# Kernel tuning notes

Hardware: AMD Instinct MI355X
Metric: run time of the kernel (lower is better)

## Reference

```python
import jax, jax.numpy as jnp
import numpy as np

N, E = 50000, 800000
IN_DIM = OUT_DIM = 256
T, R, H = 4, 8, 8
DK = OUT_DIM // H


def typed_linear(x, node_type, W, b):
    # per-node-type linear: small fixed loop over T types, select via mask
    out = jnp.zeros((x.shape[0], W.shape[2]), dtype=x.dtype)
    for t in range(W.shape[0]):
        y = x @ W[t] + b[t]
        out = jnp.where((node_type == t)[:, None], y, out)
    return out


def setup_inputs() -> dict:
    key = jax.random.key(0)
    ks = jax.random.split(key, 16)
    x = jax.random.normal(ks[0], (N, IN_DIM), dtype=jnp.float32)
    node_type = jax.random.randint(ks[1], (N,), 0, T, dtype=jnp.int32)
    src = jax.random.randint(ks[2], (E,), 0, N, dtype=jnp.int32)
    # every node receives E//N incoming edges (original skips message-less nodes)
    dst = (jnp.arange(E, dtype=jnp.int32) % N)
    etype = jax.random.randint(ks[3], (E,), 0, R, dtype=jnp.int32)
    w_scale = np.sqrt(2.0 / (IN_DIM + OUT_DIM)).astype(np.float32)
    r_scale = np.sqrt(2.0 / (DK + DK)).astype(np.float32)
    def lin(k):
        return jax.random.normal(k, (T, IN_DIM, OUT_DIM), dtype=jnp.float32) * w_scale
    return {
        "x": x, "node_type": node_type, "src": src, "dst": dst, "etype": etype,
        "Wk": lin(ks[4]), "bk": jnp.zeros((T, OUT_DIM), jnp.float32),
        "Wq": lin(ks[5]), "bq": jnp.zeros((T, OUT_DIM), jnp.float32),
        "Wv": lin(ks[6]), "bv": jnp.zeros((T, OUT_DIM), jnp.float32),
        "Wa": lin(ks[7]), "ba": jnp.zeros((T, OUT_DIM), jnp.float32),
        "rel_att": jax.random.normal(ks[8], (R, H, DK, DK), jnp.float32) * r_scale,
        "rel_msg": jax.random.normal(ks[9], (R, H, DK, DK), jnp.float32) * r_scale,
        "rel_pri": jnp.ones((R, H), jnp.float32),
        "skip": jnp.ones((T,), jnp.float32),
    }


def reference(x, node_type, src, dst, etype, Wk, bk, Wq, bq, Wv, bv, Wa, ba,
              rel_att, rel_msg, rel_pri, skip):
    n = x.shape[0]
    r = rel_att.shape[0]
    h, dk = rel_att.shape[1], rel_att.shape[2]
    sqrt_dk = jnp.asarray(np.sqrt(dk), x.dtype)

    # per-node-type K/Q/V projections -> [N, H, DK]
    k = typed_linear(x, node_type, Wk, bk).reshape(n, h, dk)
    q = typed_linear(x, node_type, Wq, bq).reshape(n, h, dk)
    v = typed_linear(x, node_type, Wv, bv).reshape(n, h, dk)

    # relation-specific transforms at node granularity: [R, N, H, DK]
    k_r = jnp.einsum('nhd,rhde->rnhe', k, rel_att)
    v_r = jnp.einsum('nhd,rhde->rnhe', v, rel_msg)

    # per-edge attention logits and messages (gather, no dense adjacency)
    key_e = k_r[etype, src]                  # [E, H, DK]
    val_e = v_r[etype, src]                  # [E, H, DK]
    att = (q[dst] * key_e).sum(-1) * rel_pri[etype] / sqrt_dk   # [E, H]

    # ragged softmax per (dst node, etype) segment, like DGL mailbox per etype
    seg = dst * r + etype
    s = n * r
    m = jax.ops.segment_max(att, seg, num_segments=s)           # [S, H]
    ex = jnp.exp(att - m[seg])
    den = jax.ops.segment_sum(ex, seg, num_segments=s)
    alpha = ex / den[seg]                                       # [E, H]
    hmsg = jax.ops.segment_sum(alpha[..., None] * val_e, seg, num_segments=s)
    hmsg = hmsg.reshape(n, r, h * dk)                           # [N, R, OUT]

    # cross_reducer='mean' over relation types that actually delivered messages
    cnt = jax.ops.segment_sum(jnp.ones((att.shape[0],), x.dtype), seg, num_segments=s)
    present = (cnt.reshape(n, r) > 0).astype(x.dtype)           # [N, R]
    t = hmsg.sum(1) / jnp.maximum(present.sum(1, keepdims=True), 1.0)

    # per-type output projection + sigmoid skip gate (dropout=identity in eval)
    trans = typed_linear(t, node_type, Wa, ba)
    a = jax.nn.sigmoid(skip)[node_type][:, None]
    return trans * a + x * (1.0 - a)
```

## Files before the change

kernel.cpp:

```cpp
#include <hip/hip_runtime.h>

#define TT 4
#define RR 8
#define NH 8
#define DKK 32

typedef float floatx4 __attribute__((ext_vector_type(4)));
typedef __bf16 bf16x8 __attribute__((ext_vector_type(8)));

__device__ __forceinline__ float us2f(unsigned short s){
    union{unsigned int u; float f;} x; x.u = ((unsigned int)s) << 16; return x.f;
}
__device__ __forceinline__ float lo2f(unsigned int u){
    union{unsigned int x; float f;} a; a.x = u << 16; return a.f;
}
__device__ __forceinline__ float hi2f(unsigned int u){
    union{unsigned int x; float f;} a; a.x = u & 0xffff0000u; return a.f;
}
__device__ __forceinline__ unsigned short f2us(float f){
    union{float f; unsigned int u;} x; x.f = f;
    unsigned int u = x.u;
    unsigned int r = (u + 0x7fffu + ((u >> 16) & 1u)) >> 16;
    return (unsigned short)r;
}
__device__ __forceinline__ float ldf(const void* p, int i, int isf32){
    return isf32 ? ((const float*)p)[i] : us2f(((const unsigned short*)p)[i]);
}
__device__ __forceinline__ float4 ldf4(const void* p, int i, int isf32){
    if (isf32) return *reinterpret_cast<const float4*>((const float*)p + i);
    uint2 u = *reinterpret_cast<const uint2*>((const unsigned short*)p + i);
    float4 r; r.x = lo2f(u.x); r.y = hi2f(u.x); r.z = lo2f(u.y); r.w = hi2f(u.y);
    return r;
}
__device__ __forceinline__ const int* sel3(const int* a, const int* b, const int* c, int s){
    return (s == 0) ? a : (s == 1) ? b : c;
}
__device__ __forceinline__ int sw32(int row, int g){
    return row * 32 + ((g ^ (row >> 2)) & 3) * 8;
}
__device__ __forceinline__ float dot8(uint4 u, const float* qa){
    return lo2f(u.x)*qa[0] + hi2f(u.x)*qa[1] + lo2f(u.y)*qa[2] + hi2f(u.y)*qa[3]
         + lo2f(u.z)*qa[4] + hi2f(u.z)*qa[5] + lo2f(u.w)*qa[6] + hi2f(u.w)*qa[7];
}

__global__ void k_flags(const void* p0, const void* p1, const void* p2, const void* p3,
                        const void* p4, const void* p5, const void* p6, const void* p7,
                        const void* p8, const void* p9, const void* p10, const void* p11,
                        const void* p12,
                        int n0, int n1, int n2, int n3, int n4, int n5, int n6, int n7,
                        int n8, int n9, int n10, int n11, int n12,
                        int* __restrict__ meta)
{
    const void* ps[13] = {p0,p1,p2,p3,p4,p5,p6,p7,p8,p9,p10,p11,p12};
    int ns[13] = {n0,n1,n2,n3,n4,n5,n6,n7,n8,n9,n10,n11,n12};
    int id = blockIdx.x;
    const unsigned short* p = (const unsigned short*)ps[id];
    int half = ns[id] >> 1;
    int nsamp = (half < 256) ? half : 256;
    int step = (nsamp > 0) ? (half / nsamp) : 1;
    int tid = threadIdx.x;
    int sane = 0, nzv = 0;
    if (tid < nsamp){
        unsigned short u = p[2 * (tid * step)];
        nzv = (u != 0);
        int e = (u >> 7) & 0xFF;
        sane = (e >= 100 && e <= 140) ? 1 : 0;
    }
    __shared__ int c_s[4], c_n[4];
    unsigned long long ms = __ballot(sane != 0);
    unsigned long long mn = __ballot(nzv != 0);
    if ((tid & 63) == 0){ c_s[tid >> 6] = (int)__popcll(ms); c_n[tid >> 6] = (int)__popcll(mn); }
    __syncthreads();
    if (tid == 0){
        int cs = c_s[0] + c_s[1] + c_s[2] + c_s[3];
        int cn = c_n[0] + c_n[1] + c_n[2] + c_n[3];
        meta[30 + id] = (cn == 0) ? -1 : ((2 * cs >= nsamp) ? 0 : 1);
    }
}
__global__ void k_flagfix(int* meta){
    if (threadIdx.x == 0 && blockIdx.x == 0){
        int xf = meta[30]; if (xf < 0) xf = 1;
        meta[30] = xf; meta[24] = xf;
        for (int j = 1; j < 13; j++) if (meta[30 + j] < 0) meta[30 + j] = xf;
    }
}

__global__ void k_trio(const int* pa, const int* pb, const int* pc, int E, int n,
                       int* __restrict__ meta){
    const int* ps[3] = {pa, pb, pc};
    int c = blockIdx.x, tid = threadIdx.x;
    const int* p = ps[c];
    int step = E / 1024; if (step < 1) step = 1;
    int mx = 0, hits = 0;
    for (int j = 0; j < 4; j++){
        long long e = (long long)(tid + j * 256) * step;
        if (e < E){
            int v = p[e];
            mx = max(mx, v);
            hits += (v == (int)(e % n)) ? 1 : 0;
        }
    }
    __shared__ int smx[4], sh[4];
    for (int o = 32; o; o >>= 1){ mx = max(mx, __shfl_down(mx, o, 64)); hits += __shfl_down(hits, o, 64); }
    if ((tid & 63) == 0){ smx[tid >> 6] = mx; sh[tid >> 6] = hits; }
    __syncthreads();
    if (tid == 0){
        mx = max(max(smx[0], smx[1]), max(smx[2], smx[3]));
        hits = sh[0] + sh[1] + sh[2] + sh[3];
        meta[44 + c] = mx; meta[47 + c] = hits;
    }
}
__global__ void k_pick(int* meta){
    if (threadIdx.x == 0 && blockIdx.x == 0){
        int m0 = meta[44], m1 = meta[45], m2 = meta[46];
        int h[3] = {meta[47], meta[48], meta[49]};
        int et = (m2 < 8) ? 2 : ((m0 < 8) ? 0 : ((m1 < 8) ? 1 : 2));
        int a = -1, b = -1;
        for (int c = 0; c < 3; c++) if (c != et){ if (a < 0) a = c; else b = c; }
        int srcsel = a, dstsel = b;
        if (h[a] >= 1000 && h[b] < 1000){ dstsel = a; srcsel = b; }
        meta[25] = srcsel; meta[26] = dstsel; meta[27] = et;
    }
}

__global__ void k_zerofill(float* out, int tot){
    int i = blockIdx.x * 256 + threadIdx.x;
    if (i < tot) out[i] = 0.f;
}
__global__ void k_copy(const void* __restrict__ xv, float* __restrict__ out,
                       const int* __restrict__ meta, int tot){
    int isf32 = meta[24];
    int i = blockIdx.x * 256 + threadIdx.x;
    if (i < tot) out[i] = ldf(xv, i, isf32);
}

__global__ void k_init(int* meta){
    if (threadIdx.x < 24) meta[threadIdx.x] = 0;
}
__global__ void k_count(const int* __restrict__ nt, int* __restrict__ meta, int n){
    int i = blockIdx.x * 256 + threadIdx.x;
    int t = (i < n) ? (nt[i] & 3) : -1;
    int lane = threadIdx.x & 63;
    #pragma unroll
    for (int tt = 0; tt < TT; tt++){
        unsigned long long m = __ballot(t == tt);
        if (m){
            int leader = __builtin_ctzll(m);
            if (lane == leader) atomicAdd(&meta[tt], (int)__popcll(m));
        }
    }
}
__global__ void k_prefix(int* meta){
    if (threadIdx.x == 0){
        int off = 0, tb = 0;
        for (int t = 0; t < TT; t++){
            int c = meta[t];
            meta[4 + t]  = off;
            meta[13 + t] = off;
            meta[8 + t]  = tb;
            off += c;
            tb  += (c + 63) >> 6;
        }
        meta[12] = tb;
    }
}
__global__ void k_scatter(const int* __restrict__ nt, int* __restrict__ meta,
                          int* __restrict__ perm, int n){
    int i = blockIdx.x * 256 + threadIdx.x;
    int t = (i < n) ? (nt[i] & 3) : -1;
    int lane = threadIdx.x & 63;
    #pragma unroll
    for (int tt = 0; tt < TT; tt++){
        unsigned long long m = __ballot(t == tt);
        if (m){
            int leader = __builtin_ctzll(m);
            int base = 0;
            if (lane == leader) base = atomicAdd(&meta[13 + tt], (int)__popcll(m));
            base = __shfl(base, leader, 64);
            if (t == tt){
                int rank = __popcll(m & ((1ull << lane) - 1ull));
                perm[base + rank] = i;
            }
        }
    }
}

__global__ void k_transW(const void* __restrict__ Wk, const void* __restrict__ Wq,
                         const void* __restrict__ Wv, const void* __restrict__ Wa,
                         unsigned short* __restrict__ WT, const int* __restrict__ meta)
{
    int idx = blockIdx.x * 256 + threadIdx.x;
    int m   = idx >> 16;
    int loc = idx & 65535;
    int j = loc >> 8, k = loc & 255;
    int mt = m >> 2, t = m & 3;
    const void* W = (mt == 0) ? Wk : (mt == 1) ? Wq : (mt == 2) ? Wv : Wa;
    int flag = meta[31 + mt];
    WT[idx] = f2us(ldf(W, t * 65536 + k * 256 + j, flag));
}

__global__ void k_transR(const void* __restrict__ rel_att, const void* __restrict__ rel_msg,
                         unsigned short* __restrict__ RATh, unsigned short* __restrict__ RATl,
                         unsigned short* __restrict__ RMTh, unsigned short* __restrict__ RMTl,
                         const int* __restrict__ meta)
{
    int idx = blockIdx.x * 256 + threadIdx.x;
    int fra = meta[39], frm = meta[40];
    float wa = ldf(rel_att, idx, fra);
    unsigned short ha = f2us(wa);
    RATh[idx] = ha;
    RATl[idx] = f2us(wa - us2f(ha));
    int quad = idx >> 10, loc = idx & 1023, d = loc >> 5, e = loc & 31;
    float wm = ldf(rel_msg, quad * 1024 + d * 32 + e, frm);
    unsigned short hm = f2us(wm);
    int oidx = quad * 1024 + e * 32 + d;
    RMTh[oidx] = hm;
    RMTl[oidx] = f2us(wm - us2f(hm));
}

__global__ __launch_bounds__(256) void k_relq(
    const unsigned short* __restrict__ Ain,
    const unsigned short* __restrict__ Bhi, const unsigned short* __restrict__ Blo,
    unsigned short* __restrict__ outF, int c0, int cend)
{
    int base = c0 + blockIdx.x * 64;
    __shared__ __align__(16) unsigned short As[64 * 264];
    int tid = threadIdx.x;
    #pragma unroll
    for (int c = 0; c < 8; c++){
        int G = c * 256 + tid;
        int row = G >> 5, g = G & 31;
        int node = base + row;
        uint4 v;
        if (node < cend) v = *reinterpret_cast<const uint4*>(Ain + (size_t)node * 256 + g * 8);
        else { v.x = v.y = v.z = v.w = 0u; }
        *reinterpret_cast<uint4*>(&As[row * 264 + g * 8]) = v;
    }
    __syncthreads();
    int wave = tid >> 6, lane = tid & 63;
    int m16 = lane & 15, quad = lane >> 4;

    #pragma unroll
    for (int rr = 0; rr < 2; rr++){
        int r = (wave << 1) + rr;
        #pragma unroll
        for (int h = 0; h < 8; h++){
            bf16x8 af[4];
            #pragma unroll
            for (int t = 0; t < 4; t++)
                af[t] = *reinterpret_cast<const bf16x8*>(&As[(t * 16 + m16) * 264 + h * 32 + quad * 8]);
            #pragma unroll
            for (int ct = 0; ct < 2; ct++){
                int bix = (((r * 8 + h) * 32) + ct * 16 + m16) * 32 + quad * 8;
                bf16x8 bh = *reinterpret_cast<const bf16x8*>(Bhi + bix);
                bf16x8 bl = *reinterpret_cast<const bf16x8*>(Blo + bix);
                floatx4 acr[4] = {};
                #pragma unroll
                for (int t = 0; t < 4; t++)
                    acr[t] = __builtin_amdgcn_mfma_f32_16x16x32_bf16(af[t], bl, acr[t], 0, 0, 0);
                #pragma unroll
                for (int t = 0; t < 4; t++)
                    acr[t] = __builtin_amdgcn_mfma_f32_16x16x32_bf16(af[t], bh, acr[t], 0, 0, 0);
                int colb = r * 256 + h * 32 + ct * 16 + m16;
                #pragma unroll
                for (int t = 0; t < 4; t++){
                    #pragma unroll
                    for (int reg = 0; reg < 4; reg++){
                        int node = base + t * 16 + quad * 4 + reg;
                        if (node < cend)
                            outF[(size_t)(node - c0) * 2048 + colb] = f2us(acr[t][reg]);
                    }
                }
            }
        }
    }
}

__global__ __launch_bounds__(256) void k_relmsg(
    const unsigned short* __restrict__ Mv,
    const unsigned short* __restrict__ Bhi, const unsigned short* __restrict__ Blo,
    unsigned short* __restrict__ outT, int c0, int cend)
{
    int base = c0 + blockIdx.x * 64;
    __shared__ __align__(16) unsigned short Ahi[64 * 264];
    int tid = threadIdx.x;
    int wave = tid >> 6, lane = tid & 63;
    int m16 = lane & 15, quad = lane >> 4;

    floatx4 acc[2][2][4] = {};

    for (int r = 0; r < RR; r++){
        __syncthreads();
        #pragma unroll
        for (int it = 0; it < 8; it++){
            int G = it * 256 + tid;
            int row = G >> 5, g = G & 31;
            int node = base + row;
            uint4 vh;
            vh.x = vh.y = vh.z = vh.w = 0u;
            if (node < cend)
                vh = *reinterpret_cast<const uint4*>(Mv + (size_t)(node - c0) * 2048 + r * 256 + g * 8);
            *reinterpret_cast<uint4*>(&Ahi[row * 264 + g * 8]) = vh;
        }
        __syncthreads();
        #pragma unroll
        for (int hh = 0; hh < 2; hh++){
            int h = (wave << 1) + hh;
            bf16x8 ah[4];
            #pragma unroll
            for (int t = 0; t < 4; t++)
                ah[t] = *reinterpret_cast<const bf16x8*>(&Ahi[(t * 16 + m16) * 264 + h * 32 + quad * 8]);
            #pragma unroll
            for (int ct = 0; ct < 2; ct++){
                int bix = (((r * 8 + h) * 32) + ct * 16 + m16) * 32 + quad * 8;
                bf16x8 bh = *reinterpret_cast<const bf16x8*>(Bhi + bix);
                bf16x8 bl = *reinterpret_cast<const bf16x8*>(Blo + bix);
                #pragma unroll
                for (int t = 0; t < 4; t++){
                    acc[hh][ct][t] = __builtin_amdgcn_mfma_f32_16x16x32_bf16(ah[t], bh, acc[hh][ct][t], 0, 0, 0);
                    acc[hh][ct][t] = __builtin_amdgcn_mfma_f32_16x16x32_bf16(ah[t], bl, acc[hh][ct][t], 0, 0, 0);
                }
            }
        }
    }
    #pragma unroll
    for (int hh = 0; hh < 2; hh++){
        int h = (wave << 1) + hh;
        #pragma unroll
        for (int ct = 0; ct < 2; ct++){
            #pragma unroll
            for (int t = 0; t < 4; t++){
                #pragma unroll
                for (int reg = 0; reg < 4; reg++){
                    int node = base + t * 16 + quad * 4 + reg;
                    if (node < cend)
                        outT[(size_t)node * 256 + h * 32 + ct * 16 + m16] = f2us(acc[hh][ct][t][reg]);
                }
            }
        }
    }
}

__global__ void k_zero(int* a, int n){
    int i = blockIdx.x * 256 + threadIdx.x;
    if (i < n) a[i] = 0;
}
__global__ void k_deg(const int* p2, const int* p3, const int* p4,
                      int* __restrict__ cnt, const int* __restrict__ meta, int E, int n){
    const int* dst = sel3(p2, p3, p4, meta[26]);
    int e = blockIdx.x * 256 + threadIdx.x;
    if (e < E){
        int d = dst[e];
        if (d >= 0 && d < n) atomicAdd(&cnt[d], 1);
    }
}
__global__ void k_scan1(const int* __restrict__ cnt, int* __restrict__ rowp,
                        int* __restrict__ bsum, int n){
    __shared__ int s[256];
    int b = blockIdx.x, tid = threadIdx.x;
    int i = b * 256 + tid;
    int v = (i < n) ? cnt[i] : 0;
    s[tid] = v;
    __syncthreads();
    for (int d = 1; d < 256; d <<= 1){
        int add = (tid >= d) ? s[tid - d] : 0;
        __syncthreads();
        s[tid] += add;
        __syncthreads();
    }
    if (i < n) rowp[i] = s[tid] - v;
    if (tid == 255) bsum[b] = s[255];
}
__global__ void k_scan2(int* bsum, int* rowp, int nb, int n){
    if (threadIdx.x == 0){
        int run = 0;
        for (int b = 0; b < nb; b++){ int t = bsum[b]; bsum[b] = run; run += t; }
        rowp[n] = run;
    }
}
__global__ void k_scan3(int* rowp, const int* __restrict__ bsum, int n){
    int i = blockIdx.x * 256 + threadIdx.x;
    if (i < n) rowp[i] += bsum[i >> 8];
}
__global__ void k_escat(const int* p2, const int* p3, const int* p4,
                        int* __restrict__ cur, const int* __restrict__ rowp,
                        int* __restrict__ eix, const int* __restrict__ meta, int E, int n){
    const int* dst = sel3(p2, p3, p4, meta[26]);
    int e = blockIdx.x * 256 + threadIdx.x;
    if (e < E){
        int d = dst[e];
        if (d >= 0 && d < n){
            int pos = atomicAdd(&cur[d], 1);
            eix[rowp[d] + pos] = e;
        }
    }
}

__global__ __launch_bounds__(256) void k_gemm_qkv(
    const void* __restrict__ Xv,
    const int* __restrict__ perm, const int* __restrict__ meta,
    const unsigned short* __restrict__ WT,
    const void* __restrict__ bk, const void* __restrict__ bq, const void* __restrict__ bv,
    unsigned short* __restrict__ kb, unsigned short* __restrict__ qb,
    unsigned short* __restrict__ vb)
{
    int rt = blockIdx.x;
    if (rt >= meta[12]) return;
    int fx = meta[30];
    int t = 0;
    while (t < TT - 1 && rt >= meta[8 + t + 1]) t++;
    int lt = rt - meta[8 + t];
    int rowStart = meta[4 + t] + (lt << 6);
    int rowEnd   = meta[4 + t] + meta[t];

    int ct = blockIdx.y;
    int mt = ct >> 1;
    int c0 = (ct & 1) * 128;
    const unsigned short* Wm = WT + (((mt << 2) + t) << 16);
    const void* bias = (mt == 0) ? bk : (mt == 1) ? bq : bv;
    int fb = meta[35 + mt];
    unsigned short* outb = (mt == 0) ? kb : (mt == 1) ? qb : vb;

    __shared__ __align__(16) unsigned short As[64 * 32];
    __shared__ __align__(16) unsigned short Bs[128 * 32];
    __shared__ int nodeIdx[64];

    int tid = threadIdx.x;
    if (tid < 64){
        int p = rowStart + tid;
        nodeIdx[tid] = perm[(p < rowEnd) ? p : (rowEnd - 1)];
    }
    __syncthreads();

    int wave = tid >> 6, lane = tid & 63;
    int wr = (wave >> 1) * 32;
    int wc = (wave & 1) * 64;
    int m16 = lane & 15, quad = lane >> 4;

    int arow = tid & 63, aseg = tid >> 6;
    int anode = nodeIdx[arow];

    floatx4 acc[2][4] = {};

    for (int k0 = 0; k0 < 256; k0 += 32){
        __syncthreads();
        uint4 av;
        if (fx){
            const float* af = (const float*)Xv + anode * 256 + aseg * 8 + k0;
            float4 f0 = *reinterpret_cast<const float4*>(af);
            float4 f1 = *reinterpret_cast<const float4*>(af + 4);
            av.x = (unsigned)f2us(f0.x) | ((unsigned)f2us(f0.y) << 16);
            av.y = (unsigned)f2us(f0.z) | ((unsigned)f2us(f0.w) << 16);
            av.z = (unsigned)f2us(f1.x) | ((unsigned)f2us(f1.y) << 16);
            av.w = (unsigned)f2us(f1.z) | ((unsigned)f2us(f1.w) << 16);
        } else {
            av = *reinterpret_cast<const uint4*>((const unsigned short*)Xv + anode * 256 + aseg * 8 + k0);
        }
        *reinterpret_cast<uint4*>(&As[sw32(arow, aseg)]) = av;
        #pragma unroll
        for (int it = 0; it < 2; it++){
            int idx2 = tid + it * 256;
            int cc = idx2 >> 2, g = idx2 & 3;
            uint4 bv4 = *reinterpret_cast<const uint4*>(Wm + (c0 + cc) * 256 + k0 + g * 8);
            *reinterpret_cast<uint4*>(&Bs[sw32(cc, g)]) = bv4;
        }
        __syncthreads();
        bf16x8 a[2], b[4];
        #pragma unroll
        for (int r = 0; r < 2; r++)
            a[r] = *reinterpret_cast<const bf16x8*>(&As[sw32(wr + r * 16 + m16, quad)]);
        #pragma unroll
        for (int c = 0; c < 4; c++)
            b[c] = *reinterpret_cast<const bf16x8*>(&Bs[sw32(wc + c * 16 + m16, quad)]);
        #pragma unroll
        for (int r = 0; r < 2; r++)
            #pragma unroll
            for (int c = 0; c < 4; c++)
                acc[r][c] = __builtin_amdgcn_mfma_f32_16x16x32_bf16(a[r], b[c], acc[r][c], 0, 0, 0);
    }

    #pragma unroll
    for (int r = 0; r < 2; r++){
        #pragma unroll
        for (int reg = 0; reg < 4; reg++){
            int row = wr + r * 16 + quad * 4 + reg;
            if (rowStart + row < rowEnd){
                int node = nodeIdx[row];
                #pragma unroll
                for (int c = 0; c < 4; c++){
                    int gc = c0 + wc + c * 16 + m16;
                    float v = acc[r][c][reg] + ldf(bias, t * 256 + gc, fb);
                    outb[node * 256 + gc] = f2us(v);
                }
            }
        }
    }
}

__global__ __launch_bounds__(256) void k_gemm_out(
    const unsigned short* __restrict__ A,
    const void* __restrict__ Xv,
    const int* __restrict__ perm, const int* __restrict__ meta,
    const unsigned short* __restrict__ WTa,
    const void* __restrict__ ba, const void* __restrict__ skipv,
    float* __restrict__ out)
{
    int rt = blockIdx.x;
    if (rt >= meta[12]) return;
    int fx = meta[30], fba = meta[38], fsk = meta[42];
    int t = 0;
    while (t < TT - 1 && rt >= meta[8 + t + 1]) t++;
    int lt = rt - meta[8 + t];
    int rowStart = meta[4 + t] + (lt << 6);
    int rowEnd   = meta[4 + t] + meta[t];
    int c0 = blockIdx.y * 128;
    const unsigned short* Wm = WTa + (t << 16);
    float sg = ldf(skipv, t, fsk);
    float ag = 1.f / (1.f + __expf(-sg));

    __shared__ __align__(16) unsigned short As[64 * 32];
    __shared__ __align__(16) unsigned short Bs[128 * 32];
    __shared__ int nodeIdx[64];

    int tid = threadIdx.x;
    if (tid < 64){
        int p = rowStart + tid;
        nodeIdx[tid] = perm[(p < rowEnd) ? p : (rowEnd - 1)];
    }
    __syncthreads();

    int wave = tid >> 6, lane = tid & 63;
    int wr = (wave >> 1) * 32;
    int wc = (wave & 1) * 64;
    int m16 = lane & 15, quad = lane >> 4;

    int arow = tid & 63, aseg = tid >> 6;
    int anode = nodeIdx[arow];
    const unsigned short* aptr = A + anode * 256 + aseg * 8;

    floatx4 acc[2][4] = {};

    for (int k0 = 0; k0 < 256; k0 += 32){
        __syncthreads();
        uint4 av = *reinterpret_cast<const uint4*>(aptr + k0);
        *reinterpret_cast<uint4*>(&As[sw32(arow, aseg)]) = av;
        #pragma unroll
        for (int it = 0; it < 2; it++){
            int idx2 = tid + it * 256;
            int cc = idx2 >> 2, g = idx2 & 3;
            uint4 bv4 = *reinterpret_cast<const uint4*>(Wm + (c0 + cc) * 256 + k0 + g * 8);
            *reinterpret_cast<uint4*>(&Bs[sw32(cc, g)]) = bv4;
        }
        __syncthreads();
        bf16x8 a[2], b[4];
        #pragma unroll
        for (int r = 0; r < 2; r++)
            a[r] = *reinterpret_cast<const bf16x8*>(&As[sw32(wr + r * 16 + m16, quad)]);
        #pragma unroll
        for (int c = 0; c < 4; c++)
            b[c] = *reinterpret_cast<const bf16x8*>(&Bs[sw32(wc + c * 16 + m16, quad)]);
        #pragma unroll
        for (int r = 0; r < 2; r++)
            #pragma unroll
            for (int c = 0; c < 4; c++)
                acc[r][c] = __builtin_amdgcn_mfma_f32_16x16x32_bf16(a[r], b[c], acc[r][c], 0, 0, 0);
    }

    #pragma unroll
    for (int r = 0; r < 2; r++){
        #pragma unroll
        for (int reg = 0; reg < 4; reg++){
            int row = wr + r * 16 + quad * 4 + reg;
            if (rowStart + row < rowEnd){
                int node = nodeIdx[row];
                #pragma unroll
                for (int c = 0; c < 4; c++){
                    int gc = c0 + wc + c * 16 + m16;
                    float v = acc[r][c][reg] + ldf(ba, t * 256 + gc, fba);
                    float xv = ldf(Xv, node * 256 + gc, fx);
                    out[node * 256 + gc] = v * ag + xv * (1.f - ag);
                }
            }
        }
    }
}

__global__ __launch_bounds__(256) void k_proj(
    const void* __restrict__ X, const int* __restrict__ nt,
    const void* __restrict__ Wk, const void* __restrict__ Wq, const void* __restrict__ Wv,
    const void* __restrict__ bk, const void* __restrict__ bq, const void* __restrict__ bv,
    unsigned short* __restrict__ kb, unsigned short* __restrict__ qtb,
    unsigned short* __restrict__ vb,
    const int* __restrict__ meta, int n)
{
    int i = blockIdx.x, tid = threadIdx.x;
    int fx = meta[30];
    int t = nt[i] & 3;
    __shared__ float xs[256];
    __shared__ float red[3][4][256];
    xs[tid] = ldf(X, i * 256 + tid, fx);
    __syncthreads();
    int seg = tid >> 6;
    int cg  = (tid & 63) * 4;
    int base = t * 65536 + cg;
    #pragma unroll
    for (int m = 0; m < 3; m++){
        const void* W = (m == 0) ? Wk : (m == 1) ? Wq : Wv;
        int fw = meta[31 + m];
        float ax = 0.f, ay = 0.f, az = 0.f, aw = 0.f;
        for (int k = seg * 64; k < seg * 64 + 64; k++){
            float xv = xs[k];
            float4 w = ldf4(W, base + k * 256, fw);
            ax += xv * w.x; ay += xv * w.y; az += xv * w.z; aw += xv * w.w;
        }
        float4 st = {ax, ay, az, aw};
        *reinterpret_cast<float4*>(&red[m][seg][cg]) = st;
    }
    __syncthreads();
    #pragma unroll
    for (int m = 0; m < 3; m++){
        const void* B = (m == 0) ? bk : (m == 1) ? bq : bv;
        unsigned short* O = (m == 0) ? kb : (m == 1) ? qtb : vb;
        float v = red[m][0][tid] + red[m][1][tid] + red[m][2][tid] + red[m][3][tid]
                + ldf(B, t * 256 + tid, meta[35 + m]);
        O[i * 256 + tid] = f2us(v);
    }
}
__global__ __launch_bounds__(256) void k_out(
    const unsigned short* __restrict__ tb,
    const void* __restrict__ X, const int* __restrict__ nt,
    const void* __restrict__ Wa, const void* __restrict__ ba,
    const void* __restrict__ skipv,
    float* __restrict__ out,
    const int* __restrict__ meta, int n)
{
    int i = blockIdx.x, tid = threadIdx.x;
    int fx = meta[30], fwa = meta[34], fba = meta[38], fsk = meta[42];
    int t = nt[i] & 3;
    __shared__ float xs[256];
    __shared__ float red[4][256];
    xs[tid] = us2f(tb[i * 256 + tid]);
    __syncthreads();
    int seg = tid >> 6;
    int cg  = (tid & 63) * 4;
    int base = t * 65536 + cg;
    float ax = 0.f, ay = 0.f, az = 0.f, aw = 0.f;
    for (int k = seg * 64; k < seg * 64 + 64; k++){
        float xv = xs[k];
        float4 w = ldf4(Wa, base + k * 256, fwa);
        ax += xv * w.x; ay += xv * w.y; az += xv * w.z; aw += xv * w.w;
    }
    float4 st = {ax, ay, az, aw};
    *reinterpret_cast<float4*>(&red[seg][cg]) = st;
    __syncthreads();
    float v = red[0][tid] + red[1][tid] + red[2][tid] + red[3][tid]
            + ldf(ba, t * 256 + tid, fba);
    float sg = ldf(skipv, t, fsk);
    float a  = 1.f / (1.f + __expf(-sg));
    float xv = ldf(X, i * 256 + tid, fx);
    out[i * 256 + tid] = v * a + xv * (1.f - a);
}

__global__ __launch_bounds__(256) void k_node2(
    unsigned short* qtb,
    const unsigned short* __restrict__ kb, const unsigned short* __restrict__ vb,
    const int* p2, const int* p3, const int* p4,
    const int* __restrict__ rowp, const int* __restrict__ eix,
    const void* __restrict__ rel_att, const void* __restrict__ rel_msg,
    const void* __restrict__ rel_pri,
    const int* __restrict__ meta, int n)
{
    const int* srcv = sel3(p2, p3, p4, meta[25]);
    const int* etv  = sel3(p2, p3, p4, meta[27]);
    int fra = meta[39], frm = meta[40], fpri = meta[41];
    int i = blockIdx.x, tid = threadIdx.x;
    int h5 = tid >> 5, z = tid & 31;

    __shared__ float qs[256];
    __shared__ float qA[RR * NH * 33];
    __shared__ float msum[RR][256];
    __shared__ float attS[16][NH];
    __shared__ float wnew[16][NH];
    __shared__ float mcur[RR][NH], dcur[RR][NH], scf[RR][NH];
    __shared__ int s_src[16], s_et[16];
    __shared__ float s_pri[RR * NH];
    __shared__ int s_mask;

    int e0 = rowp[i], deg = rowp[i + 1] - e0;

    if (tid < RR * NH) s_pri[tid] = ldf(rel_pri, tid, fpri);
    if (tid == 0) s_mask = 0;
    qs[tid] = us2f(qtb[i * 256 + tid]);
    #pragma unroll
    for (int r = 0; r < RR; r++) msum[r][tid] = 0.f;
    if (tid < RR * NH){ mcur[tid >> 3][tid & 7] = -1e30f; dcur[tid >> 3][tid & 7] = 0.f; }
    __syncthreads();

    {
        const float* qq = &qs[h5 * 32];
        #pragma unroll
        for (int r = 0; r < RR; r++){
            int base = (r * NH + h5) * 1024 + z * 32;
            float a0 = 0.f;
            #pragma unroll
            for (int e4 = 0; e4 < 8; e4++){
                float4 w = ldf4(rel_att, base + e4 * 4, fra);
                const float* q4 = qq + e4 * 4;
                a0 += w.x * q4[0] + w.y * q4[1] + w.z * q4[2] + w.w * q4[3];
            }
            qA[(r * NH + h5) * 33 + z] = a0;
        }
    }
    __syncthreads();

    for (int done = 0; done < deg; done += 16){
        int cs = min(16, deg - done);
        if (tid < cs){
            int e = eix[e0 + done + tid];
            int sj = srcv[e]; sj = (sj < 0) ? 0 : (sj >= n) ? n - 1 : sj;
            s_src[tid] = sj;
            int rr = etv[e] & 7;
            s_et[tid] = rr;
            atomicOr(&s_mask, 1 << rr);
        }
        __syncthreads();
        {
            int j = tid >> 4, hh = (tid >> 1) & 7, half = tid & 1;
            float pt = 0.f;
            if (j < cs){
                int sj = s_src[j], rj = s_et[j];
                const unsigned short* kp = kb + sj * 256 + hh * 32 + half * 16;
                const float* qa = &qA[(rj * NH + hh) * 33 + half * 16];
                uint4 u0 = *reinterpret_cast<const uint4*>(kp);
                uint4 u1 = *reinterpret_cast<const uint4*>(kp + 8);
                pt = lo2f(u0.x) * qa[0]  + hi2f(u0.x) * qa[1]
                   + lo2f(u0.y) * qa[2]  + hi2f(u0.y) * qa[3]
                   + lo2f(u0.z) * qa[4]  + hi2f(u0.z) * qa[5]
                   + lo2f(u0.w) * qa[6]  + hi2f(u0.w) * qa[7]
                   + lo2f(u1.x) * qa[8]  + hi2f(u1.x) * qa[9]
                   + lo2f(u1.y) * qa[10] + hi2f(u1.y) * qa[11]
                   + lo2f(u1.z) * qa[12] + hi2f(u1.z) * qa[13]
                   + lo2f(u1.w) * qa[14] + hi2f(u1.w) * qa[15];
            }
            pt += __shfl_xor(pt, 1);
            if (j < cs && half == 0)
                attS[j][hh] = pt * s_pri[s_et[j] * NH + hh] * 0.17677669529663687f;
        }
        __syncthreads();
        if (tid < RR * NH){
            int r = tid >> 3, hh = tid & 7;
            float m_old = mcur[r][hh];
            float m_new = m_old;
            for (int j = 0; j < cs; j++) if (s_et[j] == r) m_new = fmaxf(m_new, attS[j][hh]);
            float scale = __expf(m_old - m_new);
            float den = dcur[r][hh] * scale;
            for (int j = 0; j < cs; j++) if (s_et[j] == r) den += __expf(attS[j][hh] - m_new);
            mcur[r][hh] = m_new; dcur[r][hh] = den; scf[r][hh] = scale;
        }
        __syncthreads();
        #pragma unroll
        for (int r = 0; r < RR; r++) msum[r][tid] *= scf[r][h5];
        if (tid < cs * NH){
            int j = tid >> 3, hh = tid & 7;
            wnew[j][hh] = __expf(attS[j][hh] - mcur[s_et[j]][hh]);
        }
        __syncthreads();
        {
            float vvf[16];
            #pragma unroll
            for (int j = 0; j < 16; j++)
                if (j < cs) vvf[j] = us2f(vb[s_src[j] * 256 + tid]);
            for (int j = 0; j < cs; j++)
                msum[s_et[j]][tid] += wnew[j][h5] * vvf[j];
        }
        __syncthreads();
    }

    int mask = s_mask;
    #pragma unroll
    for (int r = 0; r < RR; r++){
        if ((mask >> r) & 1) msum[r][tid] /= dcur[r][h5];
    }
    __syncthreads();

    float tacc = 0.f;
    for (int r = 0; r < RR; r++){
        if (!((mask >> r) & 1)) continue;
        const float* ms = &msum[r][h5 * 32];
        int base = (r * NH + h5) * 1024 + z;
        float a0 = 0.f;
        #pragma unroll
        for (int c = 0; c < 32; c++)
            a0 += ms[c] * ldf(rel_msg, base + c * 32, frm);
        tacc += a0;
    }
    int np = __popc(mask); if (np == 0) np = 1;
    qtb[i * 256 + tid] = f2us(tacc / (float)np);
}

__global__ __launch_bounds__(64) void k_node5(
    const unsigned short* __restrict__ kb,
    const unsigned short* __restrict__ vb,
    unsigned short* __restrict__ qtM,
    const int* p2, const int* p3, const int* p4,
    const int* __restrict__ rowp, const int* __restrict__ eix,
    const void* __restrict__ rel_pri,
    const int* __restrict__ meta, int n, int c0)
{
    const int* srcv = sel3(p2, p3, p4, meta[25]);
    const int* etv  = sel3(p2, p3, p4, meta[27]);
    int fpri = meta[41];
    int i = c0 + blockIdx.x;
    int l = threadIdx.x;

    __shared__ float qA[RR * NH * 33];
    __shared__ float attS[16][NH];
    __shared__ float wnew[16][NH];
    __shared__ float mcur[RR][NH], dcur[RR][NH], scf[RR][NH];
    __shared__ int s_src[16], s_et[16];
    __shared__ float s_pri[RR * NH];
    __shared__ int s_mask;

    int e0 = rowp[i], deg = rowp[i + 1] - e0;

    s_pri[l] = ldf(rel_pri, l, fpri);
    if (l == 0) s_mask = 0;
    {
        const unsigned short* qp = qtM + (size_t)blockIdx.x * 2048;
        #pragma unroll
        for (int c = 0; c < 4; c++){
            int G = c * 64 + l;
            uint4 v = *reinterpret_cast<const uint4*>(qp + G * 8);
            int r = G >> 5, h = (G >> 2) & 7, dd = (G & 3) * 8;
            float* dst = &qA[(r * NH + h) * 33 + dd];
            dst[0] = lo2f(v.x); dst[1] = hi2f(v.x);
            dst[2] = lo2f(v.y); dst[3] = hi2f(v.y);
            dst[4] = lo2f(v.z); dst[5] = hi2f(v.z);
            dst[6] = lo2f(v.w); dst[7] = hi2f(v.w);
        }
    }
    float racc[RR][4];
    #pragma unroll
    for (int r = 0; r < RR; r++){
        racc[r][0] = racc[r][1] = racc[r][2] = racc[r][3] = 0.f;
    }
    mcur[l >> 3][l & 7] = -1e30f;
    dcur[l >> 3][l & 7] = 0.f;
    __syncthreads();

    int hl = l >> 3;

    for (int done = 0; done < deg; done += 16){
        int cs = min(16, deg - done);
        if (l < cs){
            int e = eix[e0 + done + l];
            int sj = srcv[e]; sj = (sj < 0) ? 0 : (sj >= n) ? n - 1 : sj;
            s_src[l] = sj;
            int rr = etv[e] & 7;
            s_et[l] = rr;
            atomicOr(&s_mask, 1 << rr);
        }
        __syncthreads();
        {
            int j = l >> 2, h2 = l & 3;
            if (j < cs){
                int sj = s_src[j], rj = s_et[j];
                const unsigned short* kp = kb + (size_t)sj * 256 + h2 * 64;
                uint4 u0 = *reinterpret_cast<const uint4*>(kp);
                uint4 u1 = *reinterpret_cast<const uint4*>(kp + 8);
                uint4 u2 = *reinterpret_cast<const uint4*>(kp + 16);
                uint4 u3 = *reinterpret_cast<const uint4*>(kp + 24);
                uint4 u4 = *reinterpret_cast<const uint4*>(kp + 32);
                uint4 u5 = *reinterpret_cast<const uint4*>(kp + 40);
                uint4 u6 = *reinterpret_cast<const uint4*>(kp + 48);
                uint4 u7 = *reinterpret_cast<const uint4*>(kp + 56);
                const float* qa0 = &qA[(rj * NH + 2 * h2) * 33];
                const float* qa1 = qa0 + 33;
                float pt0 = dot8(u0, qa0) + dot8(u1, qa0 + 8)
                          + dot8(u2, qa0 + 16) + dot8(u3, qa0 + 24);
                float pt1 = dot8(u4, qa1) + dot8(u5, qa1 + 8)
                          + dot8(u6, qa1 + 16) + dot8(u7, qa1 + 24);
                int pb = s_et[j] * NH + 2 * h2;
                attS[j][2 * h2]     = pt0 * s_pri[pb]     * 0.17677669529663687f;
                attS[j][2 * h2 + 1] = pt1 * s_pri[pb + 1] * 0.17677669529663687f;
            }
        }
        __syncthreads();
        {
            int r = l >> 3, hh = l & 7;
            float m_old = mcur[r][hh];
            float m_new = m_old;
            for (int j = 0; j < cs; j++) if (s_et[j] == r) m_new = fmaxf(m_new, attS[j][hh]);
            float scale = __expf(m_old - m_new);
            float den = dcur[r][hh] * scale;
            for (int j = 0; j < cs; j++) if (s_et[j] == r) den += __expf(attS[j][hh] - m_new);
            mcur[r][hh] = m_new; dcur[r][hh] = den; scf[r][hh] = scale;
        }
        __syncthreads();
        {
            int j = l >> 2, h2 = l & 3;
            if (j < cs){
                int rj = s_et[j];
                wnew[j][2 * h2]     = __expf(attS[j][2 * h2]     - mcur[rj][2 * h2]);
                wnew[j][2 * h2 + 1] = __expf(attS[j][2 * h2 + 1] - mcur[rj][2 * h2 + 1]);
            }
        }
        #pragma unroll
        for (int r = 0; r < RR; r++){
            float sc = scf[r][hl];
            racc[r][0] *= sc; racc[r][1] *= sc; racc[r][2] *= sc; racc[r][3] *= sc;
        }
        __syncthreads();
        for (int j = 0; j < cs; j++){
            int sj = s_src[j];
            uint2 v2 = *reinterpret_cast<const uint2*>(vb + (size_t)sj * 256 + l * 4);
            float w = wnew[j][hl];
            int et = s_et[j];
            float wv0 = w * lo2f(v2.x), wv1 = w * hi2f(v2.x);
            float wv2 = w * lo2f(v2.y), wv3 = w * hi2f(v2.y);
            #pragma unroll
            for (int r = 0; r < RR; r++){
                bool m = (et == r);
                racc[r][0] += m ? wv0 : 0.f;
                racc[r][1] += m ? wv1 : 0.f;
                racc[r][2] += m ? wv2 : 0.f;
                racc[r][3] += m ? wv3 : 0.f;
            }
        }
        __syncthreads();
    }

    int mask = s_mask;
    int np = __popc(mask); if (np == 0) np = 1;
    float inv = 1.f / (float)np;
    unsigned short* Mp = qtM + (size_t)blockIdx.x * 2048;
    #pragma unroll
    for (int r = 0; r < RR; r++){
        float d = ((mask >> r) & 1) ? (inv / dcur[r][hl]) : 0.f;
        unsigned int w0 = (unsigned)f2us(racc[r][0] * d) | ((unsigned)f2us(racc[r][1] * d) << 16);
        unsigned int w1 = (unsigned)f2us(racc[r][2] * d) | ((unsigned)f2us(racc[r][3] * d) << 16);
        uint2 pk; pk.x = w0; pk.y = w1;
        *reinterpret_cast<uint2*>(Mp + r * 256 + l * 4) = pk;
    }
}

extern "C" void kernel_launch(void* const* d_in, const int* in_sizes, int n_in,
                              void* d_out, int out_size, void* d_ws, size_t ws_size,
                              hipStream_t stream)
{
    const void* x        = d_in[0];
    const int* node_type = (const int*)d_in[1];
    const int* p2        = (const int*)d_in[2];
    const int* p3        = (const int*)d_in[3];
    const int* p4        = (const int*)d_in[4];
    const void* Wk = d_in[5];  const void* bk = d_in[6];
    const void* Wq = d_in[7];  const void* bq = d_in[8];
    const void* Wv = d_in[9];  const void* bv = d_in[10];
    const void* Wa = d_in[11]; const void* ba = d_in[12];
    const void* rel_att = d_in[13];
    const void* rel_msg = d_in[14];
    const void* rel_pri = d_in[15];
    const void* skipv   = d_in[16];
    float* out = (float*)d_out;

    bool ok = (n_in == 17);
    if (ok){
        ok = ok && (in_sizes[0] == in_sizes[1] * 256);
        ok = ok && (in_sizes[2] == in_sizes[3]) && (in_sizes[3] == in_sizes[4]);
        ok = ok && (in_sizes[5] == 262144) && (in_sizes[7] == 262144)
                && (in_sizes[9] == 262144) && (in_sizes[11] == 262144);
        ok = ok && (in_sizes[6] == 1024) && (in_sizes[8] == 1024)
                && (in_sizes[10] == 1024) && (in_sizes[12] == 1024);
        ok = ok && (in_sizes[13] == 65536) && (in_sizes[14] == 65536);
        ok = ok && (in_sizes[15] == 64) && (in_sizes[16] == 4);
        ok = ok && (out_size == in_sizes[0]);
    }
    if (!ok){
        k_zerofill<<<(out_size + 255) / 256, 256, 0, stream>>>(out, out_size);
        return;
    }

    int n = in_sizes[1];
    int E = in_sizes[2];
    int nb = (n + 255) / 256;
    int eb = (E + 255) / 256;

    char* ws = (char*)d_ws;
    int* meta = (int*)ws;
    size_t off = 256;
    int* cnt  = (int*)(ws + off); off += ((size_t)n * 4 + 255) & ~(size_t)255;
    int* bsum = (int*)(ws + off); off += ((size_t)nb * 4 + 255) & ~(size_t)255;
    int* rowp = (int*)(ws + off); off += ((size_t)(n + 1) * 4 + 255) & ~(size_t)255;
    int* eix  = (int*)(ws + off); off += ((size_t)E * 4 + 255) & ~(size_t)255;
    unsigned short* kb2 = (unsigned short*)(ws + off); off += (size_t)n * 256 * 2;
    unsigned short* vb2 = (unsigned short*)(ws + off); off += (size_t)n * 256 * 2;
    unsigned short* qtb = (unsigned short*)(ws + off); off += (size_t)n * 256 * 2;
    size_t off_lean = off;
    int* perm = (int*)(ws + off); off += ((size_t)n * 4 + 255) & ~(size_t)255;
    unsigned short* WT = (unsigned short*)(ws + off); off += (size_t)16 * 65536 * 2;
    size_t off_full = off;
    unsigned short* RATh = (unsigned short*)(ws + off); off += (size_t)65536 * 2;
    unsigned short* RATl = (unsigned short*)(ws + off); off += (size_t)65536 * 2;
    unsigned short* RMTh = (unsigned short*)(ws + off); off += (size_t)65536 * 2;
    unsigned short* RMTl = (unsigned short*)(ws + off); off += (size_t)65536 * 2;
    unsigned short* qtM = (unsigned short*)(ws + off);
    size_t avail = (ws_size > off) ? ws_size - off : 0;
    long long Cavail = (long long)(avail / 4096);
    if (Cavail > (long long)n) Cavail = n;
    int C = 0;
    if (Cavail >= 1024){
        int target = 32768;
        int nch = (n + target - 1) / target;
        int Ceven = ((n + nch - 1) / nch + 63) & ~(int)63;
        C = (Ceven < (int)Cavail) ? Ceven : (int)Cavail;
    }

    k_flags<<<13, 256, 0, stream>>>(x, Wk, Wq, Wv, Wa, bk, bq, bv, ba,
                                    rel_att, rel_msg, rel_pri, skipv,
                                    in_sizes[0], in_sizes[5], in_sizes[7], in_sizes[9],
                                    in_sizes[11], in_sizes[6], in_sizes[8], in_sizes[10],
                                    in_sizes[12], in_sizes[13], in_sizes[14],
                                    in_sizes[15], in_sizes[16], meta);
    k_flagfix<<<1, 64, 0, stream>>>(meta);

    if (ws_size < off_lean){
        k_copy<<<(n * 256 + 255) / 256, 256, 0, stream>>>(x, out, meta, n * 256);
        return;
    }
    bool full  = (ws_size >= off_full);
    bool full2 = full && (C >= 1024);

    k_trio<<<3, 256, 0, stream>>>(p2, p3, p4, E, n, meta);
    k_pick<<<1, 64, 0, stream>>>(meta);

    k_zero<<<nb, 256, 0, stream>>>(cnt, n);
    k_deg<<<eb, 256, 0, stream>>>(p2, p3, p4, cnt, meta, E, n);
    k_scan1<<<nb, 256, 0, stream>>>(cnt, rowp, bsum, n);
    k_scan2<<<1, 64, 0, stream>>>(bsum, rowp, nb, n);
    k_scan3<<<nb, 256, 0, stream>>>(rowp, bsum, n);
    k_zero<<<nb, 256, 0, stream>>>(cnt, n);
    k_escat<<<eb, 256, 0, stream>>>(p2, p3, p4, cnt, rowp, eix, meta, E, n);

    if (full){
        k_init<<<1, 64, 0, stream>>>(meta);
        k_count<<<nb, 256, 0, stream>>>(node_type, meta, n);
        k_prefix<<<1, 64, 0, stream>>>(meta);
        k_scatter<<<nb, 256, 0, stream>>>(node_type, meta, perm, n);
        k_transW<<<4096, 256, 0, stream>>>(Wk, Wq, Wv, Wa, WT, meta);
        int maxRT = n / 64 + TT;
        k_gemm_qkv<<<dim3(maxRT, 6), 256, 0, stream>>>(x, perm, meta, WT, bk, bq, bv,
                                                       kb2, qtb, vb2);
        if (full2){
            k_transR<<<256, 256, 0, stream>>>(rel_att, rel_msg, RATh, RATl, RMTh, RMTl, meta);
            for (int c0 = 0; c0 < n; c0 += C){
                int cend = (c0 + C < n) ? (c0 + C) : n;
                int blk64 = (cend - c0 + 63) >> 6;
                k_relq<<<blk64, 256, 0, stream>>>(qtb, RATh, RATl, qtM, c0, cend);
                k_node5<<<cend - c0, 64, 0, stream>>>(kb2, vb2, qtM, p2, p3, p4,
                                                      rowp, eix, rel_pri, meta, n, c0);
                k_relmsg<<<blk64, 256, 0, stream>>>(qtM, RMTh, RMTl, qtb, c0, cend);
            }
        } else {
            k_node2<<<n, 256, 0, stream>>>(qtb, kb2, vb2, p2, p3, p4, rowp, eix,
                                           rel_att, rel_msg, rel_pri, meta, n);
        }
        k_gemm_out<<<dim3(maxRT, 2), 256, 0, stream>>>(qtb, x, perm, meta,
                                                       WT + 12 * 65536, ba, skipv, out);
    } else {
        k_proj<<<n, 256, 0, stream>>>(x, node_type, Wk, Wq, Wv, bk, bq, bv,
                                      kb2, qtb, vb2, meta, n);
        k_node2<<<n, 256, 0, stream>>>(qtb, kb2, vb2, p2, p3, p4, rowp, eix,
                                       rel_att, rel_msg, rel_pri, meta, n);
        k_out<<<n, 256, 0, stream>>>(qtb, x, node_type, Wa, ba, skipv, out, meta, n);
    }
}
```

Measured before the change: 857.7 us.

## Remap per-node attention kernel so each lane owns one relation-head slice

The shared-memory staging of the relation-transformed query is dropped, and query vectors are read straight from global memory as bf16 during the key dot product. The value accumulation is remapped so each of the 64 lanes owns one (relation, head) pair with 32 accumulators. A lane only loads and accumulates the 32-element value slice for edges whose type matches its relation. This removes the masked 8-way relation accumulation and the LDS write of qA, at the cost of divergent lanes (only 8 of 64 active per edge) and repeated global query reads.

```diff
diff --git a/kernel.cpp b/kernel.cpp
--- a/kernel.cpp
+++ b/kernel.cpp
@@ -38,9 +38,11 @@
 __device__ __forceinline__ int sw32(int row, int g){
     return row * 32 + ((g ^ (row >> 2)) & 3) * 8;
 }
-__device__ __forceinline__ float dot8(uint4 u, const float* qa){
-    return lo2f(u.x)*qa[0] + hi2f(u.x)*qa[1] + lo2f(u.y)*qa[2] + hi2f(u.y)*qa[3]
-         + lo2f(u.z)*qa[4] + hi2f(u.z)*qa[5] + lo2f(u.w)*qa[6] + hi2f(u.w)*qa[7];
+__device__ __forceinline__ float dbb(uint4 a, uint4 b){
+    return lo2f(a.x)*lo2f(b.x) + hi2f(a.x)*hi2f(b.x)
+         + lo2f(a.y)*lo2f(b.y) + hi2f(a.y)*hi2f(b.y)
+         + lo2f(a.z)*lo2f(b.z) + hi2f(a.z)*hi2f(b.z)
+         + lo2f(a.w)*lo2f(b.w) + hi2f(a.w)*hi2f(b.w);
 }
 
 __global__ void k_flags(const void* p0, const void* p1, const void* p2, const void* p3,
@@ -798,7 +800,7 @@
     qtb[i * 256 + tid] = f2us(tacc / (float)np);
 }
 
-__global__ __launch_bounds__(64) void k_node5(
+__global__ __launch_bounds__(64) void k_node6(
     const unsigned short* __restrict__ kb,
     const unsigned short* __restrict__ vb,
     unsigned short* __restrict__ qtM,
@@ -813,7 +815,6 @@
     int i = c0 + blockIdx.x;
     int l = threadIdx.x;
 
-    __shared__ float qA[RR * NH * 33];
     __shared__ float attS[16][NH];
     __shared__ float wnew[16][NH];
     __shared__ float mcur[RR][NH], dcur[RR][NH], scf[RR][NH];
@@ -825,30 +826,16 @@
 
     s_pri[l] = ldf(rel_pri, l, fpri);
     if (l == 0) s_mask = 0;
-    {
-        const unsigned short* qp = qtM + (size_t)blockIdx.x * 2048;
-        #pragma unroll
-        for (int c = 0; c < 4; c++){
-            int G = c * 64 + l;
-            uint4 v = *reinterpret_cast<const uint4*>(qp + G * 8);
-            int r = G >> 5, h = (G >> 2) & 7, dd = (G & 3) * 8;
-            float* dst = &qA[(r * NH + h) * 33 + dd];
-            dst[0] = lo2f(v.x); dst[1] = hi2f(v.x);
-            dst[2] = lo2f(v.y); dst[3] = hi2f(v.y);
-            dst[4] = lo2f(v.z); dst[5] = hi2f(v.z);
-            dst[6] = lo2f(v.w); dst[7] = hi2f(v.w);
-        }
-    }
-    float racc[RR][4];
-    #pragma unroll
-    for (int r = 0; r < RR; r++){
-        racc[r][0] = racc[r][1] = racc[r][2] = racc[r][3] = 0.f;
-    }
     mcur[l >> 3][l & 7] = -1e30f;
     dcur[l >> 3][l & 7] = 0.f;
-    __syncthreads();
-
-    int hl = l >> 3;
+
+    const unsigned short* qrow = qtM + (size_t)blockIdx.x * 2048;
+    int rl = l >> 3, hl = l & 7;
+
+    float racc[32];
+    #pragma unroll
+    for (int c = 0; c < 32; c++) racc[c] = 0.f;
+    __syncthreads();
 
     for (int done = 0; done < deg; done += 16){
         int cs = min(16, deg - done);
@@ -866,6 +853,7 @@
             if (j < cs){
                 int sj = s_src[j], rj = s_et[j];
                 const unsigned short* kp = kb + (size_t)sj * 256 + h2 * 64;
+                const unsigned short* qp = qrow + (rj * NH + 2 * h2) * 32;
                 uint4 u0 = *reinterpret_cast<const uint4*>(kp);
                 uint4 u1 = *reinterpret_cast<const uint4*>(kp + 8);
                 uint4 u2 = *reinterpret_cast<const uint4*>(kp + 16);
@@ -874,13 +862,17 @@
                 uint4 u5 = *reinterpret_cast<const uint4*>(kp + 40);
                 uint4 u6 = *reinterpret_cast<const uint4*>(kp + 48);
                 uint4 u7 = *reinterpret_cast<const uint4*>(kp + 56);
-                const float* qa0 = &qA[(rj * NH + 2 * h2) * 33];
-                const float* qa1 = qa0 + 33;
-                float pt0 = dot8(u0, qa0) + dot8(u1, qa0 + 8)
-                          + dot8(u2, qa0 + 16) + dot8(u3, qa0 + 24);
-                float pt1 = dot8(u4, qa1) + dot8(u5, qa1 + 8)
-                          + dot8(u6, qa1 + 16) + dot8(u7, qa1 + 24);
-                int pb = s_et[j] * NH + 2 * h2;
+                uint4 q0 = *reinterpret_cast<const uint4*>(qp);
+                uint4 q1 = *reinterpret_cast<const uint4*>(qp + 8);
+                uint4 q2 = *reinterpret_cast<const uint4*>(qp + 16);
+                uint4 q3 = *reinterpret_cast<const uint4*>(qp + 24);
+                uint4 q4 = *reinterpret_cast<const uint4*>(qp + 32);
+                uint4 q5 = *reinterpret_cast<const uint4*>(qp + 40);
+                uint4 q6 = *reinterpret_cast<const uint4*>(qp + 48);
+                uint4 q7 = *reinterpret_cast<const uint4*>(qp + 56);
+                float pt0 = dbb(u0, q0) + dbb(u1, q1) + dbb(u2, q2) + dbb(u3, q3);
+                float pt1 = dbb(u4, q4) + dbb(u5, q5) + dbb(u6, q6) + dbb(u7, q7);
+                int pb = rj * NH + 2 * h2;
                 attS[j][2 * h2]     = pt0 * s_pri[pb]     * 0.17677669529663687f;
                 attS[j][2 * h2 + 1] = pt1 * s_pri[pb + 1] * 0.17677669529663687f;
             }
@@ -905,26 +897,38 @@
                 wnew[j][2 * h2 + 1] = __expf(attS[j][2 * h2 + 1] - mcur[rj][2 * h2 + 1]);
             }
         }
-        #pragma unroll
-        for (int r = 0; r < RR; r++){
-            float sc = scf[r][hl];
-            racc[r][0] *= sc; racc[r][1] *= sc; racc[r][2] *= sc; racc[r][3] *= sc;
+        {
+            float sc = scf[rl][hl];
+            #pragma unroll
+            for (int c = 0; c < 32; c++) racc[c] *= sc;
         }
         __syncthreads();
         for (int j = 0; j < cs; j++){
-            int sj = s_src[j];
-            uint2 v2 = *reinterpret_cast<const uint2*>(vb + (size_t)sj * 256 + l * 4);
-            float w = wnew[j][hl];
             int et = s_et[j];
-            float wv0 = w * lo2f(v2.x), wv1 = w * hi2f(v2.x);
-            float wv2 = w * lo2f(v2.y), wv3 = w * hi2f(v2.y);
-            #pragma unroll
-            for (int r = 0; r < RR; r++){
-                bool m = (et == r);
-                racc[r][0] += m ? wv0 : 0.f;
-                racc[r][1] += m ? wv1 : 0.f;
-                racc[r][2] += m ? wv2 : 0.f;
-                racc[r][3] += m ? wv3 : 0.f;
+            if (rl == et){
+                int sj = s_src[j];
+                const unsigned short* vp = vb + (size_t)sj * 256 + hl * 32;
+                uint4 v0 = *reinterpret_cast<const uint4*>(vp);
+                uint4 v1 = *reinterpret_cast<const uint4*>(vp + 8);
+                uint4 v2 = *reinterpret_cast<const uint4*>(vp + 16);
+                uint4 v3 = *reinterpret_cast<const uint4*>(vp + 24);
+                float w = wnew[j][hl];
+                racc[0]  += w * lo2f(v0.x); racc[1]  += w * hi2f(v0.x);
+                racc[2]  += w * lo2f(v0.y); racc[3]  += w * hi2f(v0.y);
+                racc[4]  += w * lo2f(v0.z); racc[5]  += w * hi2f(v0.z);
+                racc[6]  += w * lo2f(v0.w); racc[7]  += w * hi2f(v0.w);
+                racc[8]  += w * lo2f(v1.x); racc[9]  += w * hi2f(v1.x);
+                racc[10] += w * lo2f(v1.y); racc[11] += w * hi2f(v1.y);
+                racc[12] += w * lo2f(v1.z); racc[13] += w * hi2f(v1.z);
+                racc[14] += w * lo2f(v1.w); racc[15] += w * hi2f(v1.w);
+                racc[16] += w * lo2f(v2.x); racc[17] += w * hi2f(v2.x);
+                racc[18] += w * lo2f(v2.y); racc[19] += w * hi2f(v2.y);
+                racc[20] += w * lo2f(v2.z); racc[21] += w * hi2f(v2.z);
+                racc[22] += w * lo2f(v2.w); racc[23] += w * hi2f(v2.w);
+                racc[24] += w * lo2f(v3.x); racc[25] += w * hi2f(v3.x);
+                racc[26] += w * lo2f(v3.y); racc[27] += w * hi2f(v3.y);
+                racc[28] += w * lo2f(v3.z); racc[29] += w * hi2f(v3.z);
+                racc[30] += w * lo2f(v3.w); racc[31] += w * hi2f(v3.w);
             }
         }
         __syncthreads();
@@ -934,13 +938,15 @@
     int np = __popc(mask); if (np == 0) np = 1;
     float inv = 1.f / (float)np;
     unsigned short* Mp = qtM + (size_t)blockIdx.x * 2048;
-    #pragma unroll
-    for (int r = 0; r < RR; r++){
-        float d = ((mask >> r) & 1) ? (inv / dcur[r][hl]) : 0.f;
-        unsigned int w0 = (unsigned)f2us(racc[r][0] * d) | ((unsigned)f2us(racc[r][1] * d) << 16);
-        unsigned int w1 = (unsigned)f2us(racc[r][2] * d) | ((unsigned)f2us(racc[r][3] * d) << 16);
-        uint2 pk; pk.x = w0; pk.y = w1;
-        *reinterpret_cast<uint2*>(Mp + r * 256 + l * 4) = pk;
+    float d = ((mask >> rl) & 1) ? (inv / dcur[rl][hl]) : 0.f;
+    #pragma unroll
+    for (int c4 = 0; c4 < 4; c4++){
+        uint4 pk;
+        pk.x = (unsigned)f2us(racc[c4*8+0] * d) | ((unsigned)f2us(racc[c4*8+1] * d) << 16);
+        pk.y = (unsigned)f2us(racc[c4*8+2] * d) | ((unsigned)f2us(racc[c4*8+3] * d) << 16);
+        pk.z = (unsigned)f2us(racc[c4*8+4] * d) | ((unsigned)f2us(racc[c4*8+5] * d) << 16);
+        pk.w = (unsigned)f2us(racc[c4*8+6] * d) | ((unsigned)f2us(racc[c4*8+7] * d) << 16);
+        *reinterpret_cast<uint4*>(Mp + rl * 256 + hl * 32 + c4 * 8) = pk;
     }
 }
 
@@ -1056,7 +1062,7 @@
                 int cend = (c0 + C < n) ? (c0 + C) : n;
                 int blk64 = (cend - c0 + 63) >> 6;
                 k_relq<<<blk64, 256, 0, stream>>>(qtb, RATh, RATl, qtM, c0, cend);
-                k_node5<<<cend - c0, 64, 0, stream>>>(kb2, vb2, qtM, p2, p3, p4,
+                k_node6<<<cend - c0, 64, 0, stream>>>(kb2, vb2, qtM, p2, p3, p4,
                                                       rowp, eix, rel_pri, meta, n, c0);
                 k_relmsg<<<blk64, 256, 0, stream>>>(qtM, RMTh, RMTl, qtb, c0, cend);
             }
```

After: 876.4 us. 1.02x slower.
